# Kernel tuning notes

Hardware: AMD Instinct MI355X
Metric: run time of the kernel (lower is better)

Reference implementation:

```python
import jax, jax.numpy as jnp
import numpy as np

N_NODES = 100000
N_EDGES = 800000
D_IN, D_H1, D_H2, D_OUT = 512, 256, 256, 64


def setup_inputs() -> dict:
    key = jax.random.key(0)
    ks = jax.random.split(key, 8)
    x = jax.random.normal(ks[0], (N_NODES, D_IN), dtype=jnp.float32)
    edge_index = jax.random.randint(ks[1], (2, N_EDGES), 0, N_NODES, dtype=jnp.int64)
    # Glorot-style scaled weights (PyG GCNConv uses glorot init; Linear uses kaiming-uniform).
    W1 = jax.random.normal(ks[2], (D_IN, D_H1), dtype=jnp.float32) / np.sqrt(D_IN)
    b1 = jnp.zeros((D_H1,), dtype=jnp.float32)
    W2 = jax.random.normal(ks[3], (D_H1, D_H2), dtype=jnp.float32) / np.sqrt(D_H1)
    b2 = jnp.zeros((D_H2,), dtype=jnp.float32)
    Wc = jax.random.normal(ks[4], (D_H2, D_OUT), dtype=jnp.float32) / np.sqrt(D_H2)
    bc = jnp.zeros((D_OUT,), dtype=jnp.float32)
    return {"x": x, "edge_index": edge_index, "W1": W1, "b1": b1,
            "W2": W2, "b2": b2, "Wc": Wc, "bc": bc}


def reference(x, edge_index, W1, b1, W2, b2, Wc, bc):
    # GCNModel.forward in eval mode (dropout is identity when training=False).
    N = x.shape[0]
    src, dst = edge_index[0], edge_index[1]
    # PyG GCNConv: add self-loops, symmetric normalization D^-1/2 (A+I) D^-1/2.
    deg = jnp.zeros((N,), x.dtype).at[dst].add(jnp.float32(1.0)) + 1.0  # in-degree + self-loop
    dinv = jax.lax.rsqrt(deg)                         # [N]
    norm = dinv[src] * dinv[dst]                      # [E] per-edge coefficient
    self_norm = (dinv * dinv)[:, None]                # [N,1] self-loop coefficient 1/deg

    def gcn_conv(h, W, b):
        h = h @ W                                     # transform first (PyG order)
        agg = jax.ops.segment_sum(h[src] * norm[:, None], dst, num_segments=N)
        return agg + h * self_norm + b

    h = jax.nn.relu(gcn_conv(x, W1, b1))
    h = jax.nn.relu(gcn_conv(h, W2, b2))
    return h @ Wc + bc                                # [N, num_classes]
```

## Files before the change

### kernel.cpp

```cpp
#include <hip/hip_runtime.h>
#include <cstdint>

#define DIN 512
#define DH  256
#define DOUT 64

typedef __attribute__((ext_vector_type(8))) short bf16x8;
typedef __attribute__((ext_vector_type(4))) float f32x4;
typedef unsigned int uint32;

__device__ __forceinline__ unsigned short f2bf(float f) {
    uint32 u = __float_as_uint(f);
    u += 0x7fff + ((u >> 16) & 1);
    return (unsigned short)(u >> 16);
}
__device__ __forceinline__ float bf2f(unsigned short h) {
    return __uint_as_float(((uint32)h) << 16);
}
__device__ __forceinline__ float bflo(uint32 u) { return __uint_as_float(u << 16); }
__device__ __forceinline__ float bfhi(uint32 u) { return __uint_as_float(u & 0xffff0000u); }
__device__ __forceinline__ uint32 pk2(float lo, float hi) {
    return (uint32)f2bf(lo) | ((uint32)f2bf(hi) << 16);
}

__global__ void detect_i64(const unsigned long long* ei, int n_check,
                           unsigned long long bound, int* flag) {
    __shared__ int ok;
    if (threadIdx.x == 0) ok = 1;
    __syncthreads();
    int bad = 0;
    for (int i = threadIdx.x; i < n_check; i += blockDim.x) {
        if (ei[i] >= bound) bad = 1;
    }
    if (bad) ok = 0;
    __syncthreads();
    if (threadIdx.x == 0) *flag = ok;
}

__device__ __forceinline__ int get_idx(const void* ei, int is64, int pos) {
    if (is64) return (int)((const long long*)ei)[pos];
    return ((const int*)ei)[pos];
}

__global__ void count_deg(const void* ei, const int* flag, int E, int* counts) {
    const int is64 = *flag;
    int e = blockIdx.x * blockDim.x + threadIdx.x;
    if (e >= E) return;
    int d = get_idx(ei, is64, E + e);
    atomicAdd(&counts[d], 1);
}

__global__ void compute_dinv(const int* counts, float* dinv, int N) {
    int i = blockIdx.x * blockDim.x + threadIdx.x;
    if (i < N) dinv[i] = rsqrtf((float)counts[i] + 1.0f);
}

#define SCAN_BLOCK 256
#define SCAN_ELEMS 1024

__global__ void scan1(const int* counts, int* out, int* blocksums, int N) {
    __shared__ int sh[SCAN_BLOCK];
    int base = blockIdx.x * SCAN_ELEMS;
    int t = threadIdx.x;
    int v[4];
    int s = 0;
    #pragma unroll
    for (int j = 0; j < 4; j++) {
        int idx = base + t * 4 + j;
        v[j] = (idx < N) ? counts[idx] : 0;
        s += v[j];
    }
    sh[t] = s;
    __syncthreads();
    for (int off = 1; off < SCAN_BLOCK; off <<= 1) {
        int x = (t >= off) ? sh[t - off] : 0;
        __syncthreads();
        sh[t] += x;
        __syncthreads();
    }
    int run = (t == 0) ? 0 : sh[t - 1];
    #pragma unroll
    for (int j = 0; j < 4; j++) {
        int idx = base + t * 4 + j;
        if (idx < N) out[idx] = run;
        run += v[j];
    }
    if (t == SCAN_BLOCK - 1) blocksums[blockIdx.x] = sh[t];
}

__global__ void scan2(int* blocksums, int NB) {
    __shared__ int sh[SCAN_BLOCK];
    int t = threadIdx.x;
    sh[t] = (t < NB) ? blocksums[t] : 0;
    __syncthreads();
    for (int off = 1; off < SCAN_BLOCK; off <<= 1) {
        int x = (t >= off) ? sh[t - off] : 0;
        __syncthreads();
        sh[t] += x;
        __syncthreads();
    }
    if (t < NB) blocksums[t] = (t == 0) ? 0 : sh[t - 1];
}

__global__ void scan3(int* row_ptr, const int* blocksums, int N, int E) {
    int i = blockIdx.x * blockDim.x + threadIdx.x;
    if (i < N) row_ptr[i] += blocksums[i / SCAN_ELEMS];
    if (i == N) row_ptr[N] = E;
}

__global__ void fill_csr(const void* ei, const int* flag, int E,
                         const int* row_ptr, int* cursor, int* col_idx,
                         const float* dinv, float* edge_w) {
    const int is64 = *flag;
    int e = blockIdx.x * blockDim.x + threadIdx.x;
    if (e >= E) return;
    int d = get_idx(ei, is64, E + e);
    int s = get_idx(ei, is64, e);
    int pos = row_ptr[d] + atomicAdd(&cursor[d], 1);
    col_idx[pos] = s;
    edge_w[pos] = dinv[s] * dinv[d];
}

__global__ void transpose_w(const float* __restrict__ W, unsigned short* __restrict__ Bt,
                            int K, int Nw) {
    int i = blockIdx.x * blockDim.x + threadIdx.x;
    if (i >= K * Nw) return;
    int k = i / Nw, n = i % Nw;
    Bt[(size_t)n * K + k] = f2bf(W[i]);
}

template <bool A_FP32>
__global__ __launch_bounds__(256) void gemm_mfma(const void* __restrict__ Ap,
                                                 const unsigned short* __restrict__ Bt,
                                                 unsigned short* __restrict__ C,
                                                 int M, int K) {
    __shared__ unsigned short lds[20480];
    unsigned short* As = lds;
    unsigned short* Bs = lds + 4096;
    const int tid = threadIdx.x;
    const int w = tid >> 6, l = tid & 63;
    const int m0 = blockIdx.x * 64;

    f32x4 acc[4][4] = {};

    for (int k0 = 0; k0 < K; k0 += 64) {
        #pragma unroll
        for (int i = 0; i < 8; i++) {
            int row = i * 32 + (tid >> 3);
            int gq = (tid & 7) ^ (row & 7);
            const unsigned short* src = Bt + (size_t)row * K + k0 + gq * 8;
            unsigned short* dst = Bs + row * 64 + (tid & 7) * 8;
            __builtin_amdgcn_global_load_lds(
                (const __attribute__((address_space(1))) uint32*)src,
                (__attribute__((address_space(3))) uint32*)dst, 16, 0, 0);
        }
        if (A_FP32) {
            const float* Af = (const float*)Ap;
            #pragma unroll
            for (int i = 0; i < 2; i++) {
                int row = i * 32 + (tid >> 3);
                int g = tid & 7;
                int rg = m0 + row; if (rg > M - 1) rg = M - 1;
                const float* s = Af + (size_t)rg * K + k0 + g * 8;
                float4 v0 = *(const float4*)s;
                float4 v1 = *(const float4*)(s + 4);
                uint4 o;
                o.x = pk2(v0.x, v0.y); o.y = pk2(v0.z, v0.w);
                o.z = pk2(v1.x, v1.y); o.w = pk2(v1.z, v1.w);
                *(uint4*)(As + row * 64 + ((g ^ (row & 7)) * 8)) = o;
            }
        } else {
            const unsigned short* Ab = (const unsigned short*)Ap;
            #pragma unroll
            for (int i = 0; i < 2; i++) {
                int row = i * 32 + (tid >> 3);
                int gq = (tid & 7) ^ (row & 7);
                int rg = m0 + row; if (rg > M - 1) rg = M - 1;
                const unsigned short* src = Ab + (size_t)rg * K + k0 + gq * 8;
                unsigned short* dst = As + row * 64 + (tid & 7) * 8;
                __builtin_amdgcn_global_load_lds(
                    (const __attribute__((address_space(1))) uint32*)src,
                    (__attribute__((address_space(3))) uint32*)dst, 16, 0, 0);
            }
        }
        __syncthreads();
        #pragma unroll
        for (int ks = 0; ks < 2; ks++) {
            bf16x8 a[4], b[4];
            #pragma unroll
            for (int m = 0; m < 4; m++) {
                int arow = m * 16 + (l & 15);
                int ag = (ks * 4 + (l >> 4)) ^ (arow & 7);
                a[m] = *(const bf16x8*)(As + arow * 64 + ag * 8);
            }
            #pragma unroll
            for (int n = 0; n < 4; n++) {
                int brow = w * 64 + n * 16 + (l & 15);
                int bg = (ks * 4 + (l >> 4)) ^ (brow & 7);
                b[n] = *(const bf16x8*)(Bs + brow * 64 + bg * 8);
            }
            #pragma unroll
            for (int m = 0; m < 4; m++)
                #pragma unroll
                for (int n = 0; n < 4; n++)
                    acc[m][n] = __builtin_amdgcn_mfma_f32_16x16x32_bf16(a[m], b[n], acc[m][n], 0, 0, 0);
        }
        __syncthreads();
    }

    unsigned short* ep = lds + w * 4096;
    #pragma unroll
    for (int m = 0; m < 4; m++)
        #pragma unroll
        for (int n = 0; n < 4; n++)
            #pragma unroll
            for (int r = 0; r < 4; r++)
                ep[(m * 16 + (l >> 4) * 4 + r) * 64 + n * 16 + (l & 15)] = f2bf(acc[m][n][r]);
    __syncthreads();
    #pragma unroll
    for (int p = 0; p < 8; p++) {
        int row = p * 8 + (l >> 3);
        int gr = m0 + row;
        uint4 v = *(const uint4*)(ep + row * 64 + (l & 7) * 8);
        if (gr < M)
            *(uint4*)(C + (size_t)gr * 256 + w * 64 + (l & 7) * 8) = v;
    }
}

__global__ __launch_bounds__(256) void gemm_head(const unsigned short* __restrict__ A,
                                                 const unsigned short* __restrict__ Bt,
                                                 const float* __restrict__ bias,
                                                 float* __restrict__ out, int M) {
    __shared__ unsigned short As[128 * 64];
    __shared__ unsigned short Bs[64 * 64];
    const int tid = threadIdx.x;
    const int w = tid >> 6, l = tid & 63;
    const int m0 = blockIdx.x * 128;
    const int wr = w >> 1, wc = w & 1;
    f32x4 acc[4][2] = {};

    for (int k0 = 0; k0 < 256; k0 += 64) {
        #pragma unroll
        for (int i = 0; i < 4; i++) {
            int row = i * 32 + (tid >> 3);
            int gq = (tid & 7) ^ (row & 7);
            int rg = m0 + row; if (rg > M - 1) rg = M - 1;
            __builtin_amdgcn_global_load_lds(
                (const __attribute__((address_space(1))) uint32*)(A + (size_t)rg * 256 + k0 + gq * 8),
                (__attribute__((address_space(3))) uint32*)(As + row * 64 + (tid & 7) * 8), 16, 0, 0);
        }
        #pragma unroll
        for (int i = 0; i < 2; i++) {
            int row = i * 32 + (tid >> 3);
            int gq = (tid & 7) ^ (row & 7);
            __builtin_amdgcn_global_load_lds(
                (const __attribute__((address_space(1))) uint32*)(Bt + (size_t)row * 256 + k0 + gq * 8),
                (__attribute__((address_space(3))) uint32*)(Bs + row * 64 + (tid & 7) * 8), 16, 0, 0);
        }
        __syncthreads();
        #pragma unroll
        for (int ks = 0; ks < 2; ks++) {
            bf16x8 a[4], b[2];
            #pragma unroll
            for (int m = 0; m < 4; m++) {
                int arow = wr * 64 + m * 16 + (l & 15);
                int ag = (ks * 4 + (l >> 4)) ^ (arow & 7);
                a[m] = *(const bf16x8*)(As + arow * 64 + ag * 8);
            }
            #pragma unroll
            for (int n = 0; n < 2; n++) {
                int brow = wc * 32 + n * 16 + (l & 15);
                int bg = (ks * 4 + (l >> 4)) ^ (brow & 7);
                b[n] = *(const bf16x8*)(Bs + brow * 64 + bg * 8);
            }
            #pragma unroll
            for (int m = 0; m < 4; m++)
                #pragma unroll
                for (int n = 0; n < 2; n++)
                    acc[m][n] = __builtin_amdgcn_mfma_f32_16x16x32_bf16(a[m], b[n], acc[m][n], 0, 0, 0);
        }
        __syncthreads();
    }
    #pragma unroll
    for (int m = 0; m < 4; m++)
        #pragma unroll
        for (int n = 0; n < 2; n++)
            #pragma unroll
            for (int r = 0; r < 4; r++) {
                int gr = m0 + wr * 64 + m * 16 + (l >> 4) * 4 + r;
                int col = wc * 32 + n * 16 + (l & 15);
                if (gr < M) out[(size_t)gr * 64 + col] = acc[m][n][r] + bias[col];
            }
}

#define ACC8(v, wgt)                                    \
    do {                                                \
        acc[0] = fmaf(wgt, bflo(v.x), acc[0]);          \
        acc[1] = fmaf(wgt, bfhi(v.x), acc[1]);          \
        acc[2] = fmaf(wgt, bflo(v.y), acc[2]);          \
        acc[3] = fmaf(wgt, bfhi(v.y), acc[3]);          \
        acc[4] = fmaf(wgt, bflo(v.z), acc[4]);          \
        acc[5] = fmaf(wgt, bfhi(v.z), acc[5]);          \
        acc[6] = fmaf(wgt, bflo(v.w), acc[6]);          \
        acc[7] = fmaf(wgt, bfhi(v.w), acc[7]);          \
    } while (0)

__global__ __launch_bounds__(256) void aggregate_bf(const unsigned short* __restrict__ t,
                                                    const float* __restrict__ dinv,
                                                    const int* __restrict__ row_ptr,
                                                    const int* __restrict__ col_idx,
                                                    const float* __restrict__ edge_w,
                                                    const float* __restrict__ bias,
                                                    unsigned short* __restrict__ outb,
                                                    int N) {
    int wave = threadIdx.x >> 6;
    int lane = threadIdx.x & 63;
    int half = lane >> 5;
    int sl = lane & 31;
    int n = blockIdx.x * 8 + wave * 2 + half;
    if (n >= N) return;

    float dn = dinv[n];
    int r0 = row_ptr[n], r1 = row_ptr[n + 1];

    float acc[8];
    {
        uint4 sv = *(const uint4*)(t + (size_t)n * DH + sl * 8);
        float sn = dn * dn;
        acc[0] = bflo(sv.x) * sn; acc[1] = bfhi(sv.x) * sn;
        acc[2] = bflo(sv.y) * sn; acc[3] = bfhi(sv.y) * sn;
        acc[4] = bflo(sv.z) * sn; acc[5] = bfhi(sv.z) * sn;
        acc[6] = bflo(sv.w) * sn; acc[7] = bfhi(sv.w) * sn;
    }

    int j = r0;
    for (; j + 4 <= r1; j += 4) {
        int s0 = col_idx[j + 0], s1 = col_idx[j + 1];
        int s2 = col_idx[j + 2], s3 = col_idx[j + 3];
        float w0 = edge_w[j + 0], w1 = edge_w[j + 1];
        float w2 = edge_w[j + 2], w3 = edge_w[j + 3];
        uint4 v0 = *(const uint4*)(t + (size_t)s0 * DH + sl * 8);
        uint4 v1 = *(const uint4*)(t + (size_t)s1 * DH + sl * 8);
        uint4 v2 = *(const uint4*)(t + (size_t)s2 * DH + sl * 8);
        uint4 v3 = *(const uint4*)(t + (size_t)s3 * DH + sl * 8);
        ACC8(v0, w0); ACC8(v1, w1); ACC8(v2, w2); ACC8(v3, w3);
    }
    for (; j < r1; j++) {
        int s = col_idx[j];
        float wgt = edge_w[j];
        uint4 v = *(const uint4*)(t + (size_t)s * DH + sl * 8);
        ACC8(v, wgt);
    }

    float4 b0 = *(const float4*)(bias + sl * 8);
    float4 b1v = *(const float4*)(bias + sl * 8 + 4);
    acc[0] = fmaxf(acc[0] + b0.x, 0.f);  acc[1] = fmaxf(acc[1] + b0.y, 0.f);
    acc[2] = fmaxf(acc[2] + b0.z, 0.f);  acc[3] = fmaxf(acc[3] + b0.w, 0.f);
    acc[4] = fmaxf(acc[4] + b1v.x, 0.f); acc[5] = fmaxf(acc[5] + b1v.y, 0.f);
    acc[6] = fmaxf(acc[6] + b1v.z, 0.f); acc[7] = fmaxf(acc[7] + b1v.w, 0.f);

    uint4 o;
    o.x = pk2(acc[0], acc[1]);
    o.y = pk2(acc[2], acc[3]);
    o.z = pk2(acc[4], acc[5]);
    o.w = pk2(acc[6], acc[7]);
    *(uint4*)(outb + (size_t)n * DH + sl * 8) = o;
}

extern "C" void kernel_launch(void* const* d_in, const int* in_sizes, int n_in,
                              void* d_out, int out_size, void* d_ws, size_t ws_size,
                              hipStream_t stream) {
    const float* x  = (const float*)d_in[0];
    const void*  ei = d_in[1];
    const float* W1 = (const float*)d_in[2];
    const float* b1 = (const float*)d_in[3];
    const float* W2 = (const float*)d_in[4];
    const float* b2 = (const float*)d_in[5];
    const float* Wc = (const float*)d_in[6];
    const float* bc = (const float*)d_in[7];
    float* out = (float*)d_out;

    const int N = in_sizes[0] / DIN;
    const int E = in_sizes[1] / 2;

    char* ws = (char*)d_ws;
    size_t off = 0;
    auto alloc = [&](size_t bytes) -> void* {
        off = (off + 255) & ~(size_t)255;
        void* p = ws + off;
        off += bytes;
        return p;
    };

    int*   flag      = (int*)alloc(4);
    int*   counts    = (int*)alloc((size_t)N * 4);
    int*   row_ptr   = (int*)alloc((size_t)(N + 1) * 4);
    int*   col_idx   = (int*)alloc((size_t)E * 4);
    float* edge_w    = (float*)alloc((size_t)E * 4);
    int*   blocksums = (int*)alloc(1024 * 4);
    float* dinv      = (float*)alloc((size_t)N * 4);
    unsigned short* Bt1   = (unsigned short*)alloc((size_t)DH * DIN * 2);
    unsigned short* Bt2   = (unsigned short*)alloc((size_t)DH * DH * 2);
    unsigned short* Btc   = (unsigned short*)alloc((size_t)DOUT * DH * 2);
    unsigned short* t_buf = (unsigned short*)alloc((size_t)N * DH * 2);
    unsigned short* a_buf = (unsigned short*)alloc((size_t)N * DH * 2);

    const int NB = (N + SCAN_ELEMS - 1) / SCAN_ELEMS;
    const int gM64  = (N + 63) / 64;
    const int gM128 = (N + 127) / 128;

    detect_i64<<<1, 256, 0, stream>>>((const unsigned long long*)ei, 1024,
                                      (unsigned long long)N, flag);
    transpose_w<<<(DIN * DH + 255) / 256, 256, 0, stream>>>(W1, Bt1, DIN, DH);
    transpose_w<<<(DH * DH + 255) / 256, 256, 0, stream>>>(W2, Bt2, DH, DH);
    transpose_w<<<(DH * DOUT + 255) / 256, 256, 0, stream>>>(Wc, Btc, DH, DOUT);

    hipMemsetAsync(counts, 0, (size_t)N * 4, stream);
    count_deg<<<(E + 255) / 256, 256, 0, stream>>>(ei, flag, E, counts);
    compute_dinv<<<(N + 255) / 256, 256, 0, stream>>>(counts, dinv, N);
    scan1<<<NB, SCAN_BLOCK, 0, stream>>>(counts, row_ptr, blocksums, N);
    scan2<<<1, SCAN_BLOCK, 0, stream>>>(blocksums, NB);
    scan3<<<(N + 1 + 255) / 256, 256, 0, stream>>>(row_ptr, blocksums, N, E);
    hipMemsetAsync(counts, 0, (size_t)N * 4, stream);
    fill_csr<<<(E + 255) / 256, 256, 0, stream>>>(ei, flag, E, row_ptr, counts, col_idx,
                                                  dinv, edge_w);

    gemm_mfma<true><<<gM64, 256, 0, stream>>>(x, Bt1, t_buf, N, DIN);
    aggregate_bf<<<(N + 7) / 8, 256, 0, stream>>>(t_buf, dinv, row_ptr, col_idx, edge_w, b1, a_buf, N);
    gemm_mfma<false><<<gM64, 256, 0, stream>>>(a_buf, Bt2, t_buf, N, DH);
    aggregate_bf<<<(N + 7) / 8, 256, 0, stream>>>(t_buf, dinv, row_ptr, col_idx, edge_w, b2, a_buf, N);
    gemm_head<<<gM128, 256, 0, stream>>>(a_buf, Btc, bc, out, N);
}
```

Baseline: 364.0 us.

## Enlarge GEMM tile to 128 rows with 8 waves sharing B tile

The two hidden-layer GEMMs now use 512-thread blocks, each covering 128 output rows instead of 64. The 8 waves form a 2x4 grid, so each 64x256 slice of B staged in shared memory is reused across twice as many A rows, halving B traffic per output. The epilogue is split into two phases so half the waves at a time reuse the staging area. Costs are more shared memory per block, extra barriers in the epilogue, and possibly lower occupancy.

```diff
diff --git a/kernel.cpp b/kernel.cpp
--- a/kernel.cpp
+++ b/kernel.cpp
@@ -13,9 +13,6 @@
     uint32 u = __float_as_uint(f);
     u += 0x7fff + ((u >> 16) & 1);
     return (unsigned short)(u >> 16);
-}
-__device__ __forceinline__ float bf2f(unsigned short h) {
-    return __uint_as_float(((uint32)h) << 16);
 }
 __device__ __forceinline__ float bflo(uint32 u) { return __uint_as_float(u << 16); }
 __device__ __forceinline__ float bfhi(uint32 u) { return __uint_as_float(u & 0xffff0000u); }
@@ -130,36 +127,36 @@
 }
 
 template <bool A_FP32>
-__global__ __launch_bounds__(256) void gemm_mfma(const void* __restrict__ Ap,
+__global__ __launch_bounds__(512) void gemm_mfma(const void* __restrict__ Ap,
                                                  const unsigned short* __restrict__ Bt,
                                                  unsigned short* __restrict__ C,
                                                  int M, int K) {
-    __shared__ unsigned short lds[20480];
+    __shared__ unsigned short lds[24576];
     unsigned short* As = lds;
-    unsigned short* Bs = lds + 4096;
+    unsigned short* Bs = lds + 8192;
     const int tid = threadIdx.x;
     const int w = tid >> 6, l = tid & 63;
-    const int m0 = blockIdx.x * 64;
+    const int m0 = blockIdx.x * 128;
+    const int wr = w >> 2, wc = w & 3;
 
     f32x4 acc[4][4] = {};
 
     for (int k0 = 0; k0 < K; k0 += 64) {
         #pragma unroll
-        for (int i = 0; i < 8; i++) {
-            int row = i * 32 + (tid >> 3);
-            int gq = (tid & 7) ^ (row & 7);
-            const unsigned short* src = Bt + (size_t)row * K + k0 + gq * 8;
-            unsigned short* dst = Bs + row * 64 + (tid & 7) * 8;
+        for (int i = 0; i < 4; i++) {
+            int gi = i * 512 + tid;
+            int row = gi >> 3, g = gi & 7;
+            int gs = g ^ (row & 7);
             __builtin_amdgcn_global_load_lds(
-                (const __attribute__((address_space(1))) uint32*)src,
-                (__attribute__((address_space(3))) uint32*)dst, 16, 0, 0);
+                (const __attribute__((address_space(1))) uint32*)(Bt + (size_t)row * K + k0 + gs * 8),
+                (__attribute__((address_space(3))) uint32*)(Bs + row * 64 + g * 8), 16, 0, 0);
         }
         if (A_FP32) {
             const float* Af = (const float*)Ap;
             #pragma unroll
             for (int i = 0; i < 2; i++) {
-                int row = i * 32 + (tid >> 3);
-                int g = tid & 7;
+                int gi = i * 512 + tid;
+                int row = gi >> 3, g = gi & 7;
                 int rg = m0 + row; if (rg > M - 1) rg = M - 1;
                 const float* s = Af + (size_t)rg * K + k0 + g * 8;
                 float4 v0 = *(const float4*)s;
@@ -173,14 +170,13 @@
             const unsigned short* Ab = (const unsigned short*)Ap;
             #pragma unroll
             for (int i = 0; i < 2; i++) {
-                int row = i * 32 + (tid >> 3);
-                int gq = (tid & 7) ^ (row & 7);
+                int gi = i * 512 + tid;
+                int row = gi >> 3, g = gi & 7;
+                int gs = g ^ (row & 7);
                 int rg = m0 + row; if (rg > M - 1) rg = M - 1;
-                const unsigned short* src = Ab + (size_t)rg * K + k0 + gq * 8;
-                unsigned short* dst = As + row * 64 + (tid & 7) * 8;
                 __builtin_amdgcn_global_load_lds(
-                    (const __attribute__((address_space(1))) uint32*)src,
-                    (__attribute__((address_space(3))) uint32*)dst, 16, 0, 0);
+                    (const __attribute__((address_space(1))) uint32*)(Ab + (size_t)rg * K + k0 + gs * 8),
+                    (__attribute__((address_space(3))) uint32*)(As + row * 64 + g * 8), 16, 0, 0);
             }
         }
         __syncthreads();
@@ -189,15 +185,15 @@
             bf16x8 a[4], b[4];
             #pragma unroll
             for (int m = 0; m < 4; m++) {
-                int arow = m * 16 + (l & 15);
-                int ag = (ks * 4 + (l >> 4)) ^ (arow & 7);
-                a[m] = *(const bf16x8*)(As + arow * 64 + ag * 8);
+                int ar = wr * 64 + m * 16 + (l & 15);
+                int q = (ks * 4 + (l >> 4)) ^ (ar & 7);
+                a[m] = *(const bf16x8*)(As + ar * 64 + q * 8);
             }
             #pragma unroll
             for (int n = 0; n < 4; n++) {
-                int brow = w * 64 + n * 16 + (l & 15);
-                int bg = (ks * 4 + (l >> 4)) ^ (brow & 7);
-                b[n] = *(const bf16x8*)(Bs + brow * 64 + bg * 8);
+                int br = wc * 64 + n * 16 + (l & 15);
+                int q = (ks * 4 + (l >> 4)) ^ (br & 7);
+                b[n] = *(const bf16x8*)(Bs + br * 64 + q * 8);
             }
             #pragma unroll
             for (int m = 0; m < 4; m++)
@@ -208,22 +204,30 @@
         __syncthreads();
     }
 
-    unsigned short* ep = lds + w * 4096;
+    unsigned short* ep = lds + (w & 3) * 4096;
     #pragma unroll
-    for (int m = 0; m < 4; m++)
-        #pragma unroll
-        for (int n = 0; n < 4; n++)
-            #pragma unroll
-            for (int r = 0; r < 4; r++)
-                ep[(m * 16 + (l >> 4) * 4 + r) * 64 + n * 16 + (l & 15)] = f2bf(acc[m][n][r]);
-    __syncthreads();
-    #pragma unroll
-    for (int p = 0; p < 8; p++) {
-        int row = p * 8 + (l >> 3);
-        int gr = m0 + row;
-        uint4 v = *(const uint4*)(ep + row * 64 + (l & 7) * 8);
-        if (gr < M)
-            *(uint4*)(C + (size_t)gr * 256 + w * 64 + (l & 7) * 8) = v;
+    for (int ph = 0; ph < 2; ph++) {
+        if (wr == ph) {
+            #pragma unroll
+            for (int m = 0; m < 4; m++)
+                #pragma unroll
+                for (int n = 0; n < 4; n++)
+                    #pragma unroll
+                    for (int r = 0; r < 4; r++)
+                        ep[(m * 16 + (l >> 4) * 4 + r) * 64 + n * 16 + (l & 15)] = f2bf(acc[m][n][r]);
+        }
+        __syncthreads();
+        if (wr == ph) {
+            #pragma unroll
+            for (int p = 0; p < 8; p++) {
+                int row = p * 8 + (l >> 3);
+                int gr = m0 + wr * 64 + row;
+                uint4 v = *(const uint4*)(ep + row * 64 + (l & 7) * 8);
+                if (gr < M)
+                    *(uint4*)(C + (size_t)gr * 256 + wc * 64 + (l & 7) * 8) = v;
+            }
+        }
+        __syncthreads();
     }
 }
 
@@ -406,7 +410,6 @@
     unsigned short* a_buf = (unsigned short*)alloc((size_t)N * DH * 2);
 
     const int NB = (N + SCAN_ELEMS - 1) / SCAN_ELEMS;
-    const int gM64  = (N + 63) / 64;
     const int gM128 = (N + 127) / 128;
 
     detect_i64<<<1, 256, 0, stream>>>((const unsigned long long*)ei, 1024,
@@ -425,9 +428,9 @@
     fill_csr<<<(E + 255) / 256, 256, 0, stream>>>(ei, flag, E, row_ptr, counts, col_idx,
                                                   dinv, edge_w);
 
-    gemm_mfma<true><<<gM64, 256, 0, stream>>>(x, Bt1, t_buf, N, DIN);
+    gemm_mfma<true><<<gM128, 512, 0, stream>>>(x, Bt1, t_buf, N, DIN);
     aggregate_bf<<<(N + 7) / 8, 256, 0, stream>>>(t_buf, dinv, row_ptr, col_idx, edge_w, b1, a_buf, N);
-    gemm_mfma<false><<<gM64, 256, 0, stream>>>(a_buf, Bt2, t_buf, N, DH);
+    gemm_mfma<false><<<gM128, 512, 0, stream>>>(a_buf, Bt2, t_buf, N, DH);
     aggregate_bf<<<(N + 7) / 8, 256, 0, stream>>>(t_buf, dinv, row_ptr, col_idx, edge_w, b2, a_buf, N);
     gemm_head<<<gM128, 256, 0, stream>>>(a_buf, Btc, bc, out, N);
 }
```

After: 388.0 us. +6.6%, slower.
